# Performance work log

Measured on AMD Instinct MI355X. Metric: run time of the kernel, lower is better.

## Reference

```python
import jax, jax.numpy as jnp
import numpy as np

# ---- config (from init_kwargs) ----
XBOUND = (-51.2, 51.2, 0.8)
YBOUND = (-51.2, 51.2, 0.8)
ZBOUND = (-3.0, 1.0, 0.5)
FINAL_DIM = (512, 512)   # (H, W) of raw images
XV, YV, ZV = 128, 128, 8  # voxel grid dims from bounds
EPS = 1e-6


def setup_inputs() -> dict:
    key = jax.random.key(0)
    kf, ki, ke = jax.random.split(key, 3)
    feats = jax.random.normal(kf, (2, 4, 64, 64, 64), jnp.float32)   # B,N,C,Hf,Wf (post-CamEncode)
    intrins = jax.random.normal(ki, (2, 4, 4, 4), jnp.float32)       # B,N,4,4 pix_T_cam
    extrins = jax.random.normal(ke, (2, 4, 4, 4), jnp.float32)       # B,N,4,4 cam0_T_camX
    return {"feats": feats, "intrins": intrins, "extrins": extrins}


def _safe_inverse(a):
    # rigid-transform inverse: R^T, -R^T t; last row copied through (geom.safe_inverse)
    rT = jnp.swapaxes(a[:, :3, :3], 1, 2)
    t = -jnp.einsum('bij,bj->bi', rT, a[:, :3, 3])
    top = jnp.concatenate([rT, t[:, :, None]], axis=2)
    return jnp.concatenate([top, a[:, 3:4, :]], axis=1)


def _scale_intrinsics(K, sx, sy):
    # geom.scale_intrinsics: rebuild clean 4x4 intrinsics with scaled fx,fy,x0,y0
    BN = K.shape[0]
    Kn = jnp.zeros((BN, 4, 4), K.dtype)
    Kn = Kn.at[:, 0, 0].set(K[:, 0, 0] * sx)
    Kn = Kn.at[:, 1, 1].set(K[:, 1, 1] * sy)
    Kn = Kn.at[:, 0, 2].set(K[:, 0, 2] * sx)
    Kn = Kn.at[:, 1, 2].set(K[:, 1, 2] * sy)
    Kn = Kn.at[:, 2, 2].set(1.0)
    Kn = Kn.at[:, 3, 3].set(1.0)
    return Kn


def _grid_sample_zeros(feat, x, y):
    # F.grid_sample(..., align_corners=False, padding='zeros') at pixel coords (x,y)
    # feat: (BN,C,H,W); x,y: (BN,P)
    BN, C, H, W = feat.shape
    px = x - 0.5  # unnormalized sample position (align_corners=False)
    py = y - 0.5
    x0f = jnp.floor(px); y0f = jnp.floor(py)
    wx = px - x0f; wy = py - y0f
    x0 = x0f.astype(jnp.int32); y0 = y0f.astype(jnp.int32)
    featf = feat.reshape(BN, C, H * W)

    def corner(xi, yi, w):
        valid = (xi >= 0) & (xi < W) & (yi >= 0) & (yi < H)
        idx = jnp.clip(yi, 0, H - 1) * W + jnp.clip(xi, 0, W - 1)
        g = jnp.take_along_axis(featf, idx[:, None, :], axis=2)  # (BN,C,P)
        return g * (w * valid.astype(w.dtype))[:, None, :]

    return (corner(x0, y0, (1 - wx) * (1 - wy)) + corner(x0 + 1, y0, wx * (1 - wy))
            + corner(x0, y0 + 1, (1 - wx) * wy) + corner(x0 + 1, y0 + 1, wx * wy))


def _mem_grid_cam0():
    # gridcloud3d (Z,Y,X order) mapped Mem->Ref: ref = mem*vox + MIN + vox/2
    vsx = (XBOUND[1] - XBOUND[0]) / XV
    vsy = (YBOUND[1] - YBOUND[0]) / YV
    vsz = (ZBOUND[1] - ZBOUND[0]) / ZV
    gz, gy, gx = jnp.meshgrid(jnp.arange(ZV, dtype=jnp.float32),
                              jnp.arange(YV, dtype=jnp.float32),
                              jnp.arange(XV, dtype=jnp.float32), indexing='ij')
    xc = gx * vsx + (XBOUND[0] + vsx / 2)
    yc = gy * vsy + (YBOUND[0] + vsy / 2)
    zc = gz * vsz + (ZBOUND[0] + vsz / 2)
    return jnp.stack([xc, yc, zc], axis=-1).reshape(ZV * YV * XV, 3)  # (P,3)


def reference(feats, intrins, extrins):
    B, N, C, Hf, Wf = feats.shape
    BN = B * N
    feats_ = feats.reshape(BN, C, Hf, Wf)
    K = intrins.reshape(BN, 4, 4)
    E = extrins.reshape(BN, 4, 4)

    camX_T_cam0 = _safe_inverse(E)
    sy = Hf / float(FINAL_DIM[0])
    sx = Wf / float(FINAL_DIM[1])
    featpix_T_cam = _scale_intrinsics(K, sx, sy)
    pix_T_cam0 = jnp.einsum('bij,bjk->bik', featpix_T_cam, camX_T_cam0)

    xyz_cam0 = _mem_grid_cam0()  # (P,3)

    def apply44(T, p):  # (BN,4,4) x (P,3) -> (BN,P,3)
        return jnp.einsum('bij,pj->bpi', T[:, :3, :3], p) + T[:, None, :3, 3]

    xyz_camX = apply44(camX_T_cam0, xyz_cam0)
    z = xyz_camX[..., 2]
    xyz_pix = apply44(pix_T_cam0, xyz_cam0)
    denom = jnp.maximum(xyz_pix[..., 2:3], EPS)  # clamp(min=EPS)
    x = xyz_pix[..., 0] / denom[..., 0]
    y = xyz_pix[..., 1] / denom[..., 0]

    valid = ((x > -0.5) & (x < float(Wf) - 0.5) & (y > -0.5) & (y < float(Hf) - 0.5)
             & (z > 0.0)).astype(feats.dtype)  # (BN,P)

    vals = _grid_sample_zeros(feats_, x, y) * valid[:, None, :]  # (BN,C,P)
    feat_mems = vals.reshape(B, N, C, ZV, YV, XV)

    mask = (jnp.abs(feat_mems) > 0).astype(feats.dtype)
    feat_mem = jnp.sum(feat_mems * mask, axis=1) / (EPS + jnp.sum(mask, axis=1))  # (B,C,Z,Y,X)

    feat_mem = jnp.transpose(feat_mem, (0, 1, 4, 3, 2))      # b c X Y Z (permute 0,1,4,3,2)
    out = jnp.transpose(feat_mem, (0, 1, 4, 2, 3)).reshape(B, C * ZV, XV, YV)  # b (c z) h w
    return out
```

## Files before the change

### kernel.cpp

```cpp
#include <hip/hip_runtime.h>

#define BB     2
#define NN     4
#define CC     64
#define HF     64
#define WF     64
#define XVOX   128
#define YVOX   128
#define ZVOX   8
#define BN_TOT (BB * NN)
#define FEATS_PER_BN (CC * HF * WF)
#define OUT_C_STRIDE (ZVOX * XVOX * YVOX)
#define OUT_B_STRIDE (CC * OUT_C_STRIDE)

__global__ __launch_bounds__(256) void transpose_feats_kernel(
    const float* __restrict__ in, float* __restrict__ outT) {
    __shared__ float tile[64 * 65];
    int bh = blockIdx.x;
    int bn = bh >> 6;
    int h  = bh & 63;
    int t  = threadIdx.x;

    const float* src = in + bn * FEATS_PER_BN + h * WF;
#pragma unroll
    for (int k = 0; k < 16; ++k) {
        int idx = t + k * 256;
        int c = idx >> 6;
        int w = idx & 63;
        tile[w * 65 + c] = src[c * (HF * WF) + w];
    }
    __syncthreads();
    float* dst = outT + bn * FEATS_PER_BN + h * (WF * CC);
#pragma unroll
    for (int k = 0; k < 16; ++k) {
        int idx = t + k * 256;
        int w = idx >> 6;
        int c = idx & 63;
        dst[w * CC + c] = tile[w * 65 + c];
    }
}

__global__ __launch_bounds__(256) void bev_splat_kernel(
    const float* __restrict__ featsT,
    const float* __restrict__ intrins,
    const float* __restrict__ extrins,
    float* __restrict__ out) {
    __shared__ float mats_s[NN * 12];
    __shared__ __align__(16) int   offs_s[64][NN][4];
    __shared__ __align__(16) float wgts_s[64][NN][4];
    __shared__ float tile[64 * 65];

    int blk  = blockIdx.x;
    int half = blk & 1;
    int vx   = (blk >> 1) & 127;
    int vz   = (blk >> 8) & 7;
    int b    = blk >> 11;
    int vy0  = half * 64;

    if (threadIdx.x < NN) {
        int n  = threadIdx.x;
        int bn = b * NN + n;
        const float* e = extrins + bn * 16;
        const float* k = intrins + bn * 16;
        float inv[3][4];
#pragma unroll
        for (int i = 0; i < 3; ++i) {
            inv[i][0] = e[0 * 4 + i];
            inv[i][1] = e[1 * 4 + i];
            inv[i][2] = e[2 * 4 + i];
            inv[i][3] = -(e[0 * 4 + i] * e[0 * 4 + 3] +
                          e[1 * 4 + i] * e[1 * 4 + 3] +
                          e[2 * 4 + i] * e[2 * 4 + 3]);
        }
        float fx = k[0] * 0.125f;
        float fy = k[5] * 0.125f;
        float cx = k[2] * 0.125f;
        float cy = k[6] * 0.125f;
        float* m = mats_s + n * 12;
#pragma unroll
        for (int j = 0; j < 4; ++j) {
            m[j]     = fx * inv[0][j] + cx * inv[2][j];
            m[4 + j] = fy * inv[1][j] + cy * inv[2][j];
            m[8 + j] = inv[2][j];
        }
    }
    __syncthreads();

    {
        int v  = threadIdx.x >> 2;
        int n  = threadIdx.x & 3;
        int vy = vy0 + v;
        float xc = vx * 0.8f - 50.8f;
        float yc = vy * 0.8f - 50.8f;
        float zc = vz * 0.5f - 2.75f;
        const float* M = mats_s + n * 12;
        float px = M[0] * xc + M[1] * yc + M[2]  * zc + M[3];
        float py = M[4] * xc + M[5] * yc + M[6]  * zc + M[7];
        float pz = M[8] * xc + M[9] * yc + M[10] * zc + M[11];
        float denom = fmaxf(pz, 1e-6f);
        float sx = px / denom;
        float sy = py / denom;
        bool valid = (sx > -0.5f) && (sx < (float)WF - 0.5f) &&
                     (sy > -0.5f) && (sy < (float)HF - 0.5f) && (pz > 0.0f);
        int base = (b * NN + n) * FEATS_PER_BN;
        int   o[4];
        float w[4];
        if (valid) {
            float gx = sx - 0.5f;
            float gy = sy - 0.5f;
            float x0f = floorf(gx), y0f = floorf(gy);
            float wx = gx - x0f,    wy = gy - y0f;
            int x0 = (int)x0f, y0 = (int)y0f;
            int   xs[2]  = {x0, x0 + 1};
            int   ys[2]  = {y0, y0 + 1};
            float wxs[2] = {1.0f - wx, wx};
            float wys[2] = {1.0f - wy, wy};
#pragma unroll
            for (int ky = 0; ky < 2; ++ky) {
#pragma unroll
                for (int kx = 0; kx < 2; ++kx) {
                    int kk = ky * 2 + kx;
                    int xi = xs[kx], yi = ys[ky];
                    bool cv = (xi >= 0) && (xi < WF) && (yi >= 0) && (yi < HF);
                    int xic = min(max(xi, 0), WF - 1);
                    int yic = min(max(yi, 0), HF - 1);
                    o[kk] = base + (yic * WF + xic) * CC;
                    w[kk] = cv ? (wxs[kx] * wys[ky]) : 0.0f;
                }
            }
        } else {
#pragma unroll
            for (int kk = 0; kk < 4; ++kk) { o[kk] = base; w[kk] = 0.0f; }
        }
#pragma unroll
        for (int kk = 0; kk < 4; ++kk) {
            offs_s[v][n][kk] = o[kk];
            wgts_s[v][n][kk] = w[kk];
        }
    }
    __syncthreads();

    int wave = threadIdx.x >> 6;
    int lane = threadIdx.x & 63;

    for (int i = 0; i < 16; ++i) {
        int v = wave * 16 + i;
        float num = 0.0f;
        float cnt = 0.0f;
#pragma unroll
        for (int n = 0; n < NN; ++n) {
            int4   o = *reinterpret_cast<const int4*>(&offs_s[v][n][0]);
            float4 w = *reinterpret_cast<const float4*>(&wgts_s[v][n][0]);
            float wsum = (w.x + w.y) + (w.z + w.w);
            if (wsum != 0.0f) {
                float val = w.x * featsT[o.x + lane];
                val      += w.y * featsT[o.y + lane];
                val      += w.z * featsT[o.z + lane];
                val      += w.w * featsT[o.w + lane];
                num += val;
                cnt += (val != 0.0f) ? 1.0f : 0.0f;
            }
        }
        tile[v * 65 + lane] = num / (1e-6f + cnt);
    }
    __syncthreads();

    int base = b * OUT_B_STRIDE + vz * (XVOX * YVOX) + vx * YVOX + vy0;
#pragma unroll
    for (int it = 0; it < 16; ++it) {
        int idx = threadIdx.x + it * 256;
        int c = idx >> 6;
        int v = idx & 63;
        out[base + c * OUT_C_STRIDE + v] = tile[v * 65 + c];
    }
}

extern "C" void kernel_launch(void* const* d_in, const int* in_sizes, int n_in,
                              void* d_out, int out_size, void* d_ws, size_t ws_size,
                              hipStream_t stream) {
    const float* feats   = (const float*)d_in[0];
    const float* intrins = (const float*)d_in[1];
    const float* extrins = (const float*)d_in[2];
    float* out = (float*)d_out;

    float* featsT = (float*)d_ws;

    transpose_feats_kernel<<<BN_TOT * HF, 256, 0, stream>>>(feats, featsT);

    int nblk = BB * ZVOX * XVOX * 2;
    bev_splat_kernel<<<nblk, 256, 0, stream>>>(featsT, intrins, extrins, out);
}
```

Measured before the change: 121.3 us.

## Vectorize feature gathers to float4 and swizzle block order across XCDs

```diff
diff --git a/kernel.cpp b/kernel.cpp
--- a/kernel.cpp
+++ b/kernel.cpp
@@ -50,11 +50,13 @@
     __shared__ __align__(16) float wgts_s[64][NN][4];
     __shared__ float tile[64 * 65];
 
-    int blk  = blockIdx.x;
-    int half = blk & 1;
-    int vx   = (blk >> 1) & 127;
-    int vz   = (blk >> 8) & 7;
-    int b    = blk >> 11;
+    int blk = blockIdx.x;
+    int lg  = ((blk & 7) << 9) | (blk >> 3);
+
+    int half = lg & 1;
+    int vx   = (lg >> 1) & 127;
+    int vz   = (lg >> 8) & 7;
+    int b    = lg >> 11;
     int vy0  = half * 64;
 
     if (threadIdx.x < NN) {
@@ -142,26 +144,41 @@
 
     int wave = threadIdx.x >> 6;
     int lane = threadIdx.x & 63;
-
-    for (int i = 0; i < 16; ++i) {
-        int v = wave * 16 + i;
-        float num = 0.0f;
-        float cnt = 0.0f;
+    int l16  = lane & 15;
+    int vsub = lane >> 4;
+    int coff = l16 << 2;
+
+#pragma unroll
+    for (int g = 0; g < 4; ++g) {
+        int v = wave * 16 + g * 4 + vsub;
+        float n0 = 0.f, n1 = 0.f, n2 = 0.f, n3 = 0.f;
+        float c0 = 0.f, c1 = 0.f, c2 = 0.f, c3 = 0.f;
 #pragma unroll
         for (int n = 0; n < NN; ++n) {
             int4   o = *reinterpret_cast<const int4*>(&offs_s[v][n][0]);
             float4 w = *reinterpret_cast<const float4*>(&wgts_s[v][n][0]);
             float wsum = (w.x + w.y) + (w.z + w.w);
-            if (wsum != 0.0f) {
-                float val = w.x * featsT[o.x + lane];
-                val      += w.y * featsT[o.y + lane];
-                val      += w.z * featsT[o.z + lane];
-                val      += w.w * featsT[o.w + lane];
-                num += val;
-                cnt += (val != 0.0f) ? 1.0f : 0.0f;
+            if (__any(wsum != 0.0f)) {
+                float4 ga = *reinterpret_cast<const float4*>(featsT + o.x + coff);
+                float4 gb = *reinterpret_cast<const float4*>(featsT + o.y + coff);
+                float4 gc = *reinterpret_cast<const float4*>(featsT + o.z + coff);
+                float4 gd = *reinterpret_cast<const float4*>(featsT + o.w + coff);
+                float v0 = w.x * ga.x; v0 += w.y * gb.x; v0 += w.z * gc.x; v0 += w.w * gd.x;
+                float v1 = w.x * ga.y; v1 += w.y * gb.y; v1 += w.z * gc.y; v1 += w.w * gd.y;
+                float v2 = w.x * ga.z; v2 += w.y * gb.z; v2 += w.z * gc.z; v2 += w.w * gd.z;
+                float v3 = w.x * ga.w; v3 += w.y * gb.w; v3 += w.z * gc.w; v3 += w.w * gd.w;
+                n0 += v0; n1 += v1; n2 += v2; n3 += v3;
+                c0 += (v0 != 0.0f) ? 1.0f : 0.0f;
+                c1 += (v1 != 0.0f) ? 1.0f : 0.0f;
+                c2 += (v2 != 0.0f) ? 1.0f : 0.0f;
+                c3 += (v3 != 0.0f) ? 1.0f : 0.0f;
             }
         }
-        tile[v * 65 + lane] = num / (1e-6f + cnt);
+        float* tr = tile + v * 65 + coff;
+        tr[0] = n0 / (1e-6f + c0);
+        tr[1] = n1 / (1e-6f + c1);
+        tr[2] = n2 / (1e-6f + c2);
+        tr[3] = n3 / (1e-6f + c3);
     }
     __syncthreads();
 
```

Result: faster. 100.4 us (-17.3%).
